# Performance work log

Measured on AMD Instinct MI355X. Metric: run time of the kernel, lower is better.

## Reference

```python
import jax, jax.numpy as jnp
import numpy as np

D_MODEL = 1024
N_HEAD = 16


def setup_inputs() -> dict:
    key = jax.random.key(0)
    ks = jax.random.split(key, 11)
    B, S, D = 2, 2048, D_MODEL
    scale = 1.0 / np.sqrt(D)
    inp = {
        "query_tensor": jax.random.normal(ks[0], (B, S, D), jnp.float32),
        "key_tensor": jax.random.normal(ks[1], (B, S, D), jnp.float32),
        "value_tensor": jax.random.normal(ks[2], (B, S, D), jnp.float32),
        "w_q": jax.random.normal(ks[3], (D, D), jnp.float32) * scale,
        "b_q": jnp.zeros((D,), jnp.float32),
        "w_k": jax.random.normal(ks[4], (D, D), jnp.float32) * scale,
        "b_k": jnp.zeros((D,), jnp.float32),
        "w_v": jax.random.normal(ks[5], (D, D), jnp.float32) * scale,
        "b_v": jnp.zeros((D,), jnp.float32),
        "w_out": jax.random.normal(ks[6], (D, D), jnp.float32) * scale,
        "b_out": jnp.zeros((D,), jnp.float32),
    }
    return inp


def _split_heads(x, n_head):
    b, s, d = x.shape
    return x.reshape(b, s, n_head, d // n_head).transpose(0, 2, 1, 3)  # [b,h,s,dk]


def reference(query_tensor, key_tensor, value_tensor, w_q, b_q, w_k, b_k, w_v, b_v, w_out, b_out):
    # torch Linear: y = x @ W.T + b
    q = query_tensor @ w_q.T + b_q
    k = key_tensor @ w_k.T + b_k
    v = value_tensor @ w_v.T + b_v
    q = _split_heads(q, N_HEAD)
    k = _split_heads(k, N_HEAD)
    v = _split_heads(v, N_HEAD)
    d_k = k.shape[-1]
    scores = jnp.einsum("bhqd,bhkd->bhqk", q, k) / jnp.sqrt(jnp.float32(d_k))
    attn = jax.nn.softmax(scores, axis=-1)
    ctx = jnp.einsum("bhqk,bhkd->bhqd", attn, v)
    b, h, s, dk = ctx.shape
    ctx = ctx.transpose(0, 2, 1, 3).reshape(b, s, h * dk)
    return ctx @ w_out.T + b_out
```

## Files before the change

### kernel.cpp

```cpp
#include <hip/hip_runtime.h>
#include <hip/hip_bf16.h>

using ushort = unsigned short;

typedef __attribute__((ext_vector_type(8))) short bf16x8;
typedef __attribute__((ext_vector_type(4))) float f32x4;
typedef __attribute__((ext_vector_type(16))) float f32x16;
typedef __attribute__((ext_vector_type(4))) unsigned short u16x4;

#define DEVINL __device__ __forceinline__


static constexpr size_t XQ_O = 0;
static constexpr size_t WQ_O = 12582912;
static constexpr size_t WO_O = 15728640;
static constexpr size_t QB_O = 16777216;
static constexpr size_t KB_O = 20971520;
static constexpr size_t VT_O = 25165824;
static constexpr size_t CTX_O = 0;

DEVINL ushort f2bf(float f) {
  unsigned u = __builtin_bit_cast(unsigned, f);
  u += 0x7fffu + ((u >> 16) & 1u);
  return (ushort)(u >> 16);
}

DEVINL void gld16(const ushort* g, ushort* lds) {
  __builtin_amdgcn_global_load_lds(
      (const __attribute__((address_space(1))) void*)g,
      (__attribute__((address_space(3))) void*)lds, 16, 0, 0);
}

__global__ __launch_bounds__(256) void cvt_all(
    const float* __restrict__ xq, const float* __restrict__ xk, const float* __restrict__ xv,
    const float* __restrict__ wq, const float* __restrict__ wk, const float* __restrict__ wv,
    const float* __restrict__ wo, ushort* __restrict__ ws)
{
  int e = (blockIdx.x * 256 + threadIdx.x) * 8;
  const float* s;
  if      (e < 4194304)  s = xq + e;
  else if (e < 8388608)  s = xk + (e - 4194304);
  else if (e < 12582912) s = xv + (e - 8388608);
  else if (e < 13631488) s = wq + (e - 12582912);
  else if (e < 14680064) s = wk + (e - 13631488);
  else if (e < 15728640) s = wv + (e - 14680064);
  else                   s = wo + (e - 15728640);
  float4 a = *(const float4*)s;
  float4 b = *(const float4*)(s + 4);
  union { u16x4 v; ushort u[4]; } r0, r1;
  r0.u[0] = f2bf(a.x); r0.u[1] = f2bf(a.y); r0.u[2] = f2bf(a.z); r0.u[3] = f2bf(a.w);
  r1.u[0] = f2bf(b.x); r1.u[1] = f2bf(b.y); r1.u[2] = f2bf(b.z); r1.u[3] = f2bf(b.w);
  *(u16x4*)(ws + e) = r0.v;
  *(u16x4*)(ws + e + 4) = r1.v;
}

template<int BN>
DEVINL void gemm_core(const ushort* __restrict__ A, const ushort* __restrict__ Bw,
                      const float* __restrict__ bias, void* __restrict__ Cout,
                      float scale, int omode, int row0, int col0)
{
  constexpr int K = 1024;
  constexpr int BI = BN / 32;
  constexpr int NJ = BN / 32;
  __shared__ ushort As[128 * 64];
  __shared__ ushort Bs[BN * 64];
  const int t = threadIdx.x;
  const int l = t & 63;
  const int w = t >> 6;
  const int wr = w >> 1, wc = w & 1;

  const int srow = t >> 3;
  const int scol8 = (t & 7) * 8;
  const int swz_half = ((((t & 7) * 16) ^ ((srow & 7) << 4)) >> 1);

  const ushort* Ap = A + (size_t)(row0 + srow) * K + scol8;
  const ushort* Bp = Bw + (size_t)(col0 + srow) * K + scol8;

  bf16x8 areg[4], breg[BI];
  auto loadstage = [&](int k0) {
#pragma unroll
    for (int i = 0; i < 4; ++i)
      areg[i] = *(const bf16x8*)(Ap + (size_t)(i * 32) * K + k0);
#pragma unroll
    for (int i = 0; i < BI; ++i)
      breg[i] = *(const bf16x8*)(Bp + (size_t)(i * 32) * K + k0);
  };

  f32x4 acc[4][NJ];
#pragma unroll
  for (int i = 0; i < 4; ++i)
#pragma unroll
    for (int j = 0; j < NJ; ++j) acc[i][j] = (f32x4){0.f, 0.f, 0.f, 0.f};

  loadstage(0);
#pragma unroll 1
  for (int kt = 0; kt < K / 64; ++kt) {
    __syncthreads();
#pragma unroll
    for (int i = 0; i < 4; ++i)
      *(bf16x8*)&As[(srow + i * 32) * 64 + swz_half] = areg[i];
#pragma unroll
    for (int i = 0; i < BI; ++i)
      *(bf16x8*)&Bs[(srow + i * 32) * 64 + swz_half] = breg[i];
    if (kt + 1 < K / 64) loadstage((kt + 1) * 64);
    __syncthreads();
#pragma unroll
    for (int ks = 0; ks < 2; ++ks) {
      bf16x8 af[4], bfr[NJ];
#pragma unroll
      for (int mi = 0; mi < 4; ++mi) {
        int r = wr * 64 + mi * 16 + (l & 15);
        int cb = ((ks << 6) | ((l >> 4) << 4)) ^ ((r & 7) << 4);
        af[mi] = *(const bf16x8*)&As[r * 64 + (cb >> 1)];
      }
#pragma unroll
      for (int nj = 0; nj < NJ; ++nj) {
        int r = wc * (BN / 2) + nj * 16 + (l & 15);
        int cb = ((ks << 6) | ((l >> 4) << 4)) ^ ((r & 7) << 4);
        bfr[nj] = *(const bf16x8*)&Bs[r * 64 + (cb >> 1)];
      }
#pragma unroll
      for (int mi = 0; mi < 4; ++mi)
#pragma unroll
        for (int nj = 0; nj < NJ; ++nj)
          acc[mi][nj] = __builtin_amdgcn_mfma_f32_16x16x32_bf16(af[mi], bfr[nj], acc[mi][nj], 0, 0, 0);
    }
  }

  const int cl = l & 15;
#pragma unroll
  for (int mi = 0; mi < 4; ++mi) {
#pragma unroll
    for (int nj = 0; nj < NJ; ++nj) {
      int n = col0 + wc * (BN / 2) + nj * 16 + cl;
      float bv = bias[n];
      int mbase = row0 + wr * 64 + mi * 16 + (l >> 4) * 4;
      if (omode == 1) {
        float* Of = (float*)Cout;
#pragma unroll
        for (int ri = 0; ri < 4; ++ri)
          Of[(size_t)(mbase + ri) * 1024 + n] = (acc[mi][nj][ri] + bv) * scale;
      } else if (omode == 0) {
        ushort* Ob = (ushort*)Cout;
        int h = n >> 6, d = n & 63;
#pragma unroll
        for (int ri = 0; ri < 4; ++ri) {
          int m = mbase + ri;
          int b = m >> 11, s = m & 2047;
          Ob[(size_t)((b * 16 + h) * 2048 + s) * 64 + d] = f2bf((acc[mi][nj][ri] + bv) * scale);
        }
      } else {
        ushort* Ob = (ushort*)Cout;
        int h = n >> 6, d = n & 63;
        int b = mbase >> 11, s = mbase & 2047;
        union { u16x4 v; ushort u[4]; } pk;
#pragma unroll
        for (int ri = 0; ri < 4; ++ri) pk.u[ri] = f2bf((acc[mi][nj][ri] + bv) * scale);
        *(u16x4*)&Ob[(size_t)((b * 16 + h) * 64 + d) * 2048 + s] = pk.v;
      }
    }
  }
}

__global__ __launch_bounds__(256, 2) void gemm_qkv(
    const ushort* __restrict__ ws_c, ushort* __restrict__ ws_m,
    const float* __restrict__ bq, const float* __restrict__ bk, const float* __restrict__ bv)
{
  const int z = blockIdx.z;
  const ushort* A = ws_c + XQ_O + (size_t)z * 4194304;
  const ushort* W = ws_c + WQ_O + (size_t)z * 1048576;
  const float* bias = (z == 0) ? bq : ((z == 1) ? bk : bv);
  ushort* dst = ws_m + QB_O + (size_t)z * 4194304;
  float scale = (z == 0) ? (0.125f * 1.4426950408889634f) : 1.0f;
  int omode = (z == 2) ? 2 : 0;
  gemm_core<128>(A, W, bias, dst, scale, omode, blockIdx.y * 128, blockIdx.x * 128);
}

__global__ __launch_bounds__(256, 2) void gemm_out(
    const ushort* __restrict__ ctx, const ushort* __restrict__ wo,
    const float* __restrict__ bo, float* __restrict__ out)
{
  gemm_core<64>(ctx, wo, bo, out, 1.0f, 1, blockIdx.y * 128, blockIdx.x * 64);
}

__global__ __launch_bounds__(512, 4) void attn8(
    const ushort* __restrict__ Qb, const ushort* __restrict__ Kb,
    const ushort* __restrict__ Vtb, ushort* __restrict__ Ctx)
{
  __shared__ ushort smem[32768];

  const int t = threadIdx.x, l = t & 63, w = t >> 6;
  const int wq4 = w & 3, half = w >> 2;
  const int hi2 = l >> 5, q = l & 31;

  const int hw = blockIdx.y * 16 + blockIdx.x;
  const int j = hw >> 3;
  const int bh = (hw & 7) + 8 * (j >> 4);
  const int qt = j & 15;

  const int kvb = half * 1024;
  const ushort* Qp = Qb + ((size_t)bh * 2048 + qt * 128 + wq4 * 32) * 64;
  const ushort* Kp = Kb + (size_t)bh * 2048 * 64;
  const ushort* Vp = Vtb + (size_t)bh * 64 * 2048;

  ushort* Ksh = smem + half * 8192;
  ushort* Vsh = smem + 16384 + half * 8192;

  bf16x8 qf[4];
#pragma unroll
  for (int ks = 0; ks < 4; ++ks)
    qf[ks] = *(const bf16x8*)(Qp + q * 64 + ks * 16 + hi2 * 8);

  auto stageKV = [&](int pp, int kv0) {
#pragma unroll
    for (int i = 0; i < 2; ++i) {
      int R = (i * 4 + wq4) * 8 + (l >> 3);
      int g = l & 7;
      int sR = (R & ~12) | ((R & 4) << 1) | ((R & 8) >> 1);
      gld16(Kp + (size_t)(kv0 + sR) * 64 + (g ^ (R & 7)) * 8,
            Ksh + pp * 4096 + (i * 4 + wq4) * 512);
      gld16(Vp + (size_t)R * 2048 + kv0 + (g ^ (R & 7)) * 8,
            Vsh + pp * 4096 + (i * 4 + wq4) * 512);
    }
  };

  f32x16 acc0, acc1;
#pragma unroll
  for (int i = 0; i < 16; ++i) { acc0[i] = 0.f; acc1[i] = 0.f; }
  f32x16 Zv;
#pragma unroll
  for (int i = 0; i < 16; ++i) Zv[i] = 0.f;
  float lrun = 0.f;

  const int rsw = (q & 7) << 4;

  stageKV(0, kvb);
  __syncthreads();

#pragma unroll 1
  for (int kt = 0; kt < 16; ++kt) {
    const int p = kt & 1;
    const ushort* Kl = Ksh + p * 4096;
    const ushort* Vl = Vsh + p * 4096;

    f32x16 scA, scB;
    __builtin_amdgcn_s_setprio(1);
    {
      bf16x8 kf = *(const bf16x8*)&Kl[q * 64 + (((hi2 * 16)) ^ rsw) / 2];
      scA = __builtin_amdgcn_mfma_f32_32x32x16_bf16(kf, qf[0], Zv, 0, 0, 0);
#pragma unroll
      for (int ks = 1; ks < 4; ++ks) {
        bf16x8 k2 = *(const bf16x8*)&Kl[q * 64 + (((ks * 32 + hi2 * 16) ^ rsw) >> 1)];
        scA = __builtin_amdgcn_mfma_f32_32x32x16_bf16(k2, qf[ks], scA, 0, 0, 0);
      }
      const int r1 = (32 + q) * 64;
      bf16x8 kg = *(const bf16x8*)&Kl[r1 + (((hi2 * 16)) ^ rsw) / 2];
      scB = __builtin_amdgcn_mfma_f32_32x32x16_bf16(kg, qf[0], Zv, 0, 0, 0);
#pragma unroll
      for (int ks = 1; ks < 4; ++ks) {
        bf16x8 k2 = *(const bf16x8*)&Kl[r1 + (((ks * 32 + hi2 * 16) ^ rsw) >> 1)];
        scB = __builtin_amdgcn_mfma_f32_32x32x16_bf16(k2, qf[ks], scB, 0, 0, 0);
      }
    }
    __builtin_amdgcn_s_setprio(0);

    if (kt + 1 < 16) stageKV(p ^ 1, kvb + (kt + 1) * 64);

#pragma unroll
    for (int c = 0; c < 2; ++c) {
      f32x16& sc = (c == 0) ? scA : scB;
      float s0 = 0.f, s1 = 0.f, s2 = 0.f, s3 = 0.f;
#pragma unroll
      for (int i = 0; i < 4; ++i) {
        float e0 = __builtin_amdgcn_exp2f(sc[i]);      sc[i] = e0;      s0 += e0;
        float e1 = __builtin_amdgcn_exp2f(sc[4 + i]);  sc[4 + i] = e1;  s1 += e1;
        float e2 = __builtin_amdgcn_exp2f(sc[8 + i]);  sc[8 + i] = e2;  s2 += e2;
        float e3 = __builtin_amdgcn_exp2f(sc[12 + i]); sc[12 + i] = e3; s3 += e3;
      }
      lrun += (s0 + s1) + (s2 + s3);

      union PU { bf16x8 v; unsigned u[4]; } pA, pB;
#pragma unroll
      for (int i = 0; i < 4; ++i) {
        asm("v_cvt_pk_bf16_f32 %0, %1, %2" : "=v"(pA.u[i]) : "v"(sc[2 * i]), "v"(sc[2 * i + 1]));
        asm("v_cvt_pk_bf16_f32 %0, %1, %2" : "=v"(pB.u[i]) : "v"(sc[8 + 2 * i]), "v"(sc[9 + 2 * i]));
      }

      __builtin_amdgcn_s_setprio(1);
#pragma unroll
      for (int db = 0; db < 2; ++db) {
        const int d = db * 32 + q;
        bf16x8 va = *(const bf16x8*)&Vl[d * 64 + (((c * 64 + hi2 * 16) ^ rsw) >> 1)];
        bf16x8 vb = *(const bf16x8*)&Vl[d * 64 + (((c * 64 + 32 + hi2 * 16) ^ rsw) >> 1)];
        if (db == 0) {
          acc0 = __builtin_amdgcn_mfma_f32_32x32x16_bf16(va, pA.v, acc0, 0, 0, 0);
          acc0 = __builtin_amdgcn_mfma_f32_32x32x16_bf16(vb, pB.v, acc0, 0, 0, 0);
        } else {
          acc1 = __builtin_amdgcn_mfma_f32_32x32x16_bf16(va, pA.v, acc1, 0, 0, 0);
          acc1 = __builtin_amdgcn_mfma_f32_32x32x16_bf16(vb, pB.v, acc1, 0, 0, 0);
        }
      }
      __builtin_amdgcn_s_setprio(0);
    }
    __syncthreads();
  }

  float lsum = lrun + __shfl_xor(lrun, 32);
  float* Lf = (float*)smem;

  if (l < 32) Lf[half * 128 + wq4 * 32 + q] = lsum;
  __syncthreads();
  const float inv = 1.0f / (Lf[wq4 * 32 + q] + Lf[128 + wq4 * 32 + q]);
  __syncthreads();

  auto mrg = [&](int row, int G) -> float* {
    return Lf + row * 64 + ((G ^ (row & 15)) << 2);
  };

  if (half == 1) {
    const int row = wq4 * 32 + q;
#pragma unroll
    for (int db = 0; db < 2; ++db)
#pragma unroll
      for (int g = 0; g < 4; ++g) {
        float4 v;
        if (db == 0) v = (float4){acc0[g * 4], acc0[g * 4 + 1], acc0[g * 4 + 2], acc0[g * 4 + 3]};
        else         v = (float4){acc1[g * 4], acc1[g * 4 + 1], acc1[g * 4 + 2], acc1[g * 4 + 3]};
        *(float4*)mrg(row, db * 8 + g * 2 + hi2) = v;
      }
  }
  __syncthreads();

  if (half == 0) {
    const int row = wq4 * 32 + q;
#pragma unroll
    for (int db = 0; db < 2; ++db)
#pragma unroll
      for (int g = 0; g < 4; ++g) {
        float* p = mrg(row, db * 8 + g * 2 + hi2);
        float4 pv = *(float4*)p;
        float4 o;
        if (db == 0) o = (float4){(acc0[g * 4] + pv.x) * inv, (acc0[g * 4 + 1] + pv.y) * inv,
                                  (acc0[g * 4 + 2] + pv.z) * inv, (acc0[g * 4 + 3] + pv.w) * inv};
        else         o = (float4){(acc1[g * 4] + pv.x) * inv, (acc1[g * 4 + 1] + pv.y) * inv,
                                  (acc1[g * 4 + 2] + pv.z) * inv, (acc1[g * 4 + 3] + pv.w) * inv};
        *(float4*)p = o;
      }
  }
  __syncthreads();

  {
    const int b = bh >> 4, h = bh & 15;
    const int d0 = (l & 7) * 8;
#pragma unroll
    for (int rr = 0; rr < 2; ++rr) {
      int row = w * 16 + rr * 8 + (l >> 3);
      float4 f0 = *(const float4*)mrg(row, (l & 7) * 2);
      float4 f1 = *(const float4*)mrg(row, (l & 7) * 2 + 1);
      union { u16x4 v; ushort u[4]; } o0, o1;
      o0.u[0] = f2bf(f0.x); o0.u[1] = f2bf(f0.y); o0.u[2] = f2bf(f0.z); o0.u[3] = f2bf(f0.w);
      o1.u[0] = f2bf(f1.x); o1.u[1] = f2bf(f1.y); o1.u[2] = f2bf(f1.z); o1.u[3] = f2bf(f1.w);
      ushort* dst = Ctx + ((size_t)b * 2048 + qt * 128 + row) * 1024 + h * 64 + d0;
      *(u16x4*)dst = o0.v;
      *(u16x4*)(dst + 4) = o1.v;
    }
  }
}

extern "C" void kernel_launch(void* const* d_in, const int* in_sizes, int n_in,
                              void* d_out, int out_size, void* d_ws, size_t ws_size,
                              hipStream_t stream) {
  const float* xq = (const float*)d_in[0];
  const float* xk = (const float*)d_in[1];
  const float* xv = (const float*)d_in[2];
  const float* wq = (const float*)d_in[3];
  const float* bq = (const float*)d_in[4];
  const float* wk = (const float*)d_in[5];
  const float* bk = (const float*)d_in[6];
  const float* wv = (const float*)d_in[7];
  const float* bv = (const float*)d_in[8];
  const float* wo = (const float*)d_in[9];
  const float* bo = (const float*)d_in[10];
  ushort* ws = (ushort*)d_ws;

  cvt_all<<<8192, 256, 0, stream>>>(xq, xk, xv, wq, wk, wv, wo, ws);
  gemm_qkv<<<dim3(8, 32, 3), 256, 0, stream>>>(ws, ws, bq, bk, bv);
  attn8<<<dim3(16, 32), 512, 0, stream>>>(ws + QB_O, ws + KB_O, ws + VT_O, ws + CTX_O);
  gemm_out<<<dim3(16, 32), 256, 0, stream>>>(ws + CTX_O, ws + WO_O, bo, (float*)d_out);
}
```

Measured before the change: 114.4 us.

## Restructure attention into 4-way KV split with 64 query rows per wave

The attention kernel now splits the KV sequence four ways across waves, and each wave handles 64 query rows (two 32-row MFMA tiles) instead of 32. Each K/V fragment read from LDS is therefore reused across two query tiles, which halves LDS reads per MFMA. K and V staging is divided between wave groups, with one loading K and the other loading V. This doubles LDS use to 128KB and the accumulator registers, so occupancy drops to 2 blocks per CU, and the final merge of four partial results takes more steps and barriers.

```diff
diff --git a/kernel.cpp b/kernel.cpp
--- a/kernel.cpp
+++ b/kernel.cpp
@@ -183,14 +183,14 @@
   gemm_core<64>(ctx, wo, bo, out, 1.0f, 1, blockIdx.y * 128, blockIdx.x * 64);
 }
 
-__global__ __launch_bounds__(512, 4) void attn8(
+__global__ __launch_bounds__(512, 2) void attn4k(
     const ushort* __restrict__ Qb, const ushort* __restrict__ Kb,
     const ushort* __restrict__ Vtb, ushort* __restrict__ Ctx)
 {
-  __shared__ ushort smem[32768];
+  __shared__ ushort smem[65536];
 
   const int t = threadIdx.x, l = t & 63, w = t >> 6;
-  const int wq4 = w & 3, half = w >> 2;
+  const int kq = w & 3, qw = w >> 2;
   const int hi2 = l >> 5, q = l & 31;
 
   const int hw = blockIdx.y * 16 + blockIdx.x;
@@ -198,92 +198,98 @@
   const int bh = (hw & 7) + 8 * (j >> 4);
   const int qt = j & 15;
 
-  const int kvb = half * 1024;
-  const ushort* Qp = Qb + ((size_t)bh * 2048 + qt * 128 + wq4 * 32) * 64;
+  const ushort* Qp = Qb + ((size_t)bh * 2048 + qt * 128 + qw * 64) * 64;
   const ushort* Kp = Kb + (size_t)bh * 2048 * 64;
   const ushort* Vp = Vtb + (size_t)bh * 64 * 2048;
 
-  ushort* Ksh = smem + half * 8192;
-  ushort* Vsh = smem + 16384 + half * 8192;
-
-  bf16x8 qf[4];
-#pragma unroll
-  for (int ks = 0; ks < 4; ++ks)
-    qf[ks] = *(const bf16x8*)(Qp + q * 64 + ks * 16 + hi2 * 8);
-
-  auto stageKV = [&](int pp, int kv0) {
-#pragma unroll
-    for (int i = 0; i < 2; ++i) {
-      int R = (i * 4 + wq4) * 8 + (l >> 3);
-      int g = l & 7;
-      int sR = (R & ~12) | ((R & 4) << 1) | ((R & 8) >> 1);
-      gld16(Kp + (size_t)(kv0 + sR) * 64 + (g ^ (R & 7)) * 8,
-            Ksh + pp * 4096 + (i * 4 + wq4) * 512);
-      gld16(Vp + (size_t)R * 2048 + kv0 + (g ^ (R & 7)) * 8,
-            Vsh + pp * 4096 + (i * 4 + wq4) * 512);
+  ushort* Ksh = smem + kq * 8192;
+  ushort* Vsh = smem + 32768 + kq * 8192;
+
+  bf16x8 qf[2][4];
+#pragma unroll
+  for (int qs = 0; qs < 2; ++qs)
+#pragma unroll
+    for (int ks = 0; ks < 4; ++ks)
+      qf[qs][ks] = *(const bf16x8*)(Qp + (qs * 32 + q) * 64 + ks * 16 + hi2 * 8);
+
+  auto stage = [&](int pp, int kv0) {
+    if (qw == 0) {
+#pragma unroll
+      for (int i = 0; i < 8; ++i) {
+        int R = i * 8 + (l >> 3);
+        int g = l & 7;
+        int sR = (R & ~12) | ((R & 4) << 1) | ((R & 8) >> 1);
+        gld16(Kp + (size_t)(kv0 + sR) * 64 + (g ^ (R & 7)) * 8,
+              Ksh + pp * 4096 + i * 512);
+      }
+    } else {
+#pragma unroll
+      for (int i = 0; i < 8; ++i) {
+        int R = i * 8 + (l >> 3);
+        int g = l & 7;
+        gld16(Vp + (size_t)R * 2048 + kv0 + (g ^ (R & 7)) * 8,
+              Vsh + pp * 4096 + i * 512);
+      }
     }
   };
 
-  f32x16 acc0, acc1;
-#pragma unroll
-  for (int i = 0; i < 16; ++i) { acc0[i] = 0.f; acc1[i] = 0.f; }
+  f32x16 acc[4];
   f32x16 Zv;
 #pragma unroll
   for (int i = 0; i < 16; ++i) Zv[i] = 0.f;
-  float lrun = 0.f;
+#pragma unroll
+  for (int a = 0; a < 4; ++a) acc[a] = Zv;
+  float lr0 = 0.f, lr1 = 0.f;
 
   const int rsw = (q & 7) << 4;
-
-  stageKV(0, kvb);
+  const int kvq = kq * 512;
+
+  stage(0, kvq);
   __syncthreads();
 
 #pragma unroll 1
-  for (int kt = 0; kt < 16; ++kt) {
+  for (int kt = 0; kt < 8; ++kt) {
     const int p = kt & 1;
     const ushort* Kl = Ksh + p * 4096;
     const ushort* Vl = Vsh + p * 4096;
 
-    f32x16 scA, scB;
-    __builtin_amdgcn_s_setprio(1);
-    {
-      bf16x8 kf = *(const bf16x8*)&Kl[q * 64 + (((hi2 * 16)) ^ rsw) / 2];
-      scA = __builtin_amdgcn_mfma_f32_32x32x16_bf16(kf, qf[0], Zv, 0, 0, 0);
+#pragma unroll
+    for (int c = 0; c < 2; ++c) {
+      bf16x8 kf[4];
+#pragma unroll
+      for (int ks = 0; ks < 4; ++ks)
+        kf[ks] = *(const bf16x8*)&Kl[(c * 32 + q) * 64 + (((ks * 32 + hi2 * 16) ^ rsw) >> 1)];
+      f32x16 s0, s1;
+      __builtin_amdgcn_s_setprio(1);
+      s0 = __builtin_amdgcn_mfma_f32_32x32x16_bf16(kf[0], qf[0][0], Zv, 0, 0, 0);
+      s1 = __builtin_amdgcn_mfma_f32_32x32x16_bf16(kf[0], qf[1][0], Zv, 0, 0, 0);
 #pragma unroll
       for (int ks = 1; ks < 4; ++ks) {
-        bf16x8 k2 = *(const bf16x8*)&Kl[q * 64 + (((ks * 32 + hi2 * 16) ^ rsw) >> 1)];
-        scA = __builtin_amdgcn_mfma_f32_32x32x16_bf16(k2, qf[ks], scA, 0, 0, 0);
-      }
-      const int r1 = (32 + q) * 64;
-      bf16x8 kg = *(const bf16x8*)&Kl[r1 + (((hi2 * 16)) ^ rsw) / 2];
-      scB = __builtin_amdgcn_mfma_f32_32x32x16_bf16(kg, qf[0], Zv, 0, 0, 0);
-#pragma unroll
-      for (int ks = 1; ks < 4; ++ks) {
-        bf16x8 k2 = *(const bf16x8*)&Kl[r1 + (((ks * 32 + hi2 * 16) ^ rsw) >> 1)];
-        scB = __builtin_amdgcn_mfma_f32_32x32x16_bf16(k2, qf[ks], scB, 0, 0, 0);
-      }
-    }
-    __builtin_amdgcn_s_setprio(0);
-
-    if (kt + 1 < 16) stageKV(p ^ 1, kvb + (kt + 1) * 64);
-
-#pragma unroll
-    for (int c = 0; c < 2; ++c) {
-      f32x16& sc = (c == 0) ? scA : scB;
-      float s0 = 0.f, s1 = 0.f, s2 = 0.f, s3 = 0.f;
+        s0 = __builtin_amdgcn_mfma_f32_32x32x16_bf16(kf[ks], qf[0][ks], s0, 0, 0, 0);
+        s1 = __builtin_amdgcn_mfma_f32_32x32x16_bf16(kf[ks], qf[1][ks], s1, 0, 0, 0);
+      }
+      __builtin_amdgcn_s_setprio(0);
+
+      if (c == 0 && kt < 7) stage(p ^ 1, kvq + (kt + 1) * 64);
+
+      float a0 = 0.f, a1 = 0.f, b0 = 0.f, b1 = 0.f;
+#pragma unroll
+      for (int i = 0; i < 8; ++i) {
+        float e0 = __builtin_amdgcn_exp2f(s0[i]);      s0[i] = e0;      a0 += e0;
+        float e1 = __builtin_amdgcn_exp2f(s0[8 + i]);  s0[8 + i] = e1;  a1 += e1;
+        float e2 = __builtin_amdgcn_exp2f(s1[i]);      s1[i] = e2;      b0 += e2;
+        float e3 = __builtin_amdgcn_exp2f(s1[8 + i]);  s1[8 + i] = e3;  b1 += e3;
+      }
+      lr0 += a0 + a1;
+      lr1 += b0 + b1;
+
+      union PU { bf16x8 v; unsigned u[4]; } pA0, pB0, pA1, pB1;
 #pragma unroll
       for (int i = 0; i < 4; ++i) {
-        float e0 = __builtin_amdgcn_exp2f(sc[i]);      sc[i] = e0;      s0 += e0;
-        float e1 = __builtin_amdgcn_exp2f(sc[4 + i]);  sc[4 + i] = e1;  s1 += e1;
-        float e2 = __builtin_amdgcn_exp2f(sc[8 + i]);  sc[8 + i] = e2;  s2 += e2;
-        float e3 = __builtin_amdgcn_exp2f(sc[12 + i]); sc[12 + i] = e3; s3 += e3;
-      }
-      lrun += (s0 + s1) + (s2 + s3);
-
-      union PU { bf16x8 v; unsigned u[4]; } pA, pB;
-#pragma unroll
-      for (int i = 0; i < 4; ++i) {
-        asm("v_cvt_pk_bf16_f32 %0, %1, %2" : "=v"(pA.u[i]) : "v"(sc[2 * i]), "v"(sc[2 * i + 1]));
-        asm("v_cvt_pk_bf16_f32 %0, %1, %2" : "=v"(pB.u[i]) : "v"(sc[8 + 2 * i]), "v"(sc[9 + 2 * i]));
+        asm("v_cvt_pk_bf16_f32 %0, %1, %2" : "=v"(pA0.u[i]) : "v"(s0[2 * i]), "v"(s0[2 * i + 1]));
+        asm("v_cvt_pk_bf16_f32 %0, %1, %2" : "=v"(pB0.u[i]) : "v"(s0[8 + 2 * i]), "v"(s0[9 + 2 * i]));
+        asm("v_cvt_pk_bf16_f32 %0, %1, %2" : "=v"(pA1.u[i]) : "v"(s1[2 * i]), "v"(s1[2 * i + 1]));
+        asm("v_cvt_pk_bf16_f32 %0, %1, %2" : "=v"(pB1.u[i]) : "v"(s1[8 + 2 * i]), "v"(s1[9 + 2 * i]));
       }
 
       __builtin_amdgcn_s_setprio(1);
@@ -292,75 +298,113 @@
         const int d = db * 32 + q;
         bf16x8 va = *(const bf16x8*)&Vl[d * 64 + (((c * 64 + hi2 * 16) ^ rsw) >> 1)];
         bf16x8 vb = *(const bf16x8*)&Vl[d * 64 + (((c * 64 + 32 + hi2 * 16) ^ rsw) >> 1)];
-        if (db == 0) {
-          acc0 = __builtin_amdgcn_mfma_f32_32x32x16_bf16(va, pA.v, acc0, 0, 0, 0);
-          acc0 = __builtin_amdgcn_mfma_f32_32x32x16_bf16(vb, pB.v, acc0, 0, 0, 0);
-        } else {
-          acc1 = __builtin_amdgcn_mfma_f32_32x32x16_bf16(va, pA.v, acc1, 0, 0, 0);
-          acc1 = __builtin_amdgcn_mfma_f32_32x32x16_bf16(vb, pB.v, acc1, 0, 0, 0);
+        acc[db]     = __builtin_amdgcn_mfma_f32_32x32x16_bf16(va, pA0.v, acc[db], 0, 0, 0);
+        acc[db]     = __builtin_amdgcn_mfma_f32_32x32x16_bf16(vb, pB0.v, acc[db], 0, 0, 0);
+        acc[2 + db] = __builtin_amdgcn_mfma_f32_32x32x16_bf16(va, pA1.v, acc[2 + db], 0, 0, 0);
+        acc[2 + db] = __builtin_amdgcn_mfma_f32_32x32x16_bf16(vb, pB1.v, acc[2 + db], 0, 0, 0);
+      }
+      __builtin_amdgcn_s_setprio(0);
+    }
+    __syncthreads();
+  }
+
+  float ls0 = lr0 + __shfl_xor(lr0, 32);
+  float ls1 = lr1 + __shfl_xor(lr1, 32);
+  float* Lf = (float*)smem;
+  if (l < 32) {
+    Lf[16384 + kq * 128 + qw * 64 + q] = ls0;
+    Lf[16384 + kq * 128 + qw * 64 + 32 + q] = ls1;
+  }
+  __syncthreads();
+  const float inv0 = 1.0f / (Lf[16384 + qw * 64 + q] + Lf[16384 + 128 + qw * 64 + q] +
+                             Lf[16384 + 256 + qw * 64 + q] + Lf[16384 + 384 + qw * 64 + q]);
+  const float inv1 = 1.0f / (Lf[16384 + qw * 64 + 32 + q] + Lf[16384 + 128 + qw * 64 + 32 + q] +
+                             Lf[16384 + 256 + qw * 64 + 32 + q] + Lf[16384 + 384 + qw * 64 + 32 + q]);
+  __syncthreads();
+
+  auto mrg = [&](float* base, int row, int slot) -> float* {
+    return base + row * 64 + ((slot ^ (row & 15)) << 2);
+  };
+
+  if (kq == 1 || kq == 3) {
+    float* Rg = Lf + ((kq == 1) ? 0 : 8192) + qw * 4096;
+#pragma unroll
+    for (int qs = 0; qs < 2; ++qs)
+#pragma unroll
+      for (int db = 0; db < 2; ++db)
+#pragma unroll
+        for (int g = 0; g < 4; ++g) {
+          float4 v = (float4){acc[qs * 2 + db][g * 4], acc[qs * 2 + db][g * 4 + 1],
+                              acc[qs * 2 + db][g * 4 + 2], acc[qs * 2 + db][g * 4 + 3]};
+          *(float4*)mrg(Rg, qs * 32 + q, db * 8 + g * 2 + hi2) = v;
         }
-      }
-      __builtin_amdgcn_s_setprio(0);
-    }
-    __syncthreads();
-  }
-
-  float lsum = lrun + __shfl_xor(lrun, 32);
-  float* Lf = (float*)smem;
-
-  if (l < 32) Lf[half * 128 + wq4 * 32 + q] = lsum;
-  __syncthreads();
-  const float inv = 1.0f / (Lf[wq4 * 32 + q] + Lf[128 + wq4 * 32 + q]);
-  __syncthreads();
-
-  auto mrg = [&](int row, int G) -> float* {
-    return Lf + row * 64 + ((G ^ (row & 15)) << 2);
-  };
-
-  if (half == 1) {
-    const int row = wq4 * 32 + q;
-#pragma unroll
-    for (int db = 0; db < 2; ++db)
-#pragma unroll
-      for (int g = 0; g < 4; ++g) {
-        float4 v;
-        if (db == 0) v = (float4){acc0[g * 4], acc0[g * 4 + 1], acc0[g * 4 + 2], acc0[g * 4 + 3]};
-        else         v = (float4){acc1[g * 4], acc1[g * 4 + 1], acc1[g * 4 + 2], acc1[g * 4 + 3]};
-        *(float4*)mrg(row, db * 8 + g * 2 + hi2) = v;
-      }
-  }
-  __syncthreads();
-
-  if (half == 0) {
-    const int row = wq4 * 32 + q;
-#pragma unroll
-    for (int db = 0; db < 2; ++db)
-#pragma unroll
-      for (int g = 0; g < 4; ++g) {
-        float* p = mrg(row, db * 8 + g * 2 + hi2);
-        float4 pv = *(float4*)p;
-        float4 o;
-        if (db == 0) o = (float4){(acc0[g * 4] + pv.x) * inv, (acc0[g * 4 + 1] + pv.y) * inv,
-                                  (acc0[g * 4 + 2] + pv.z) * inv, (acc0[g * 4 + 3] + pv.w) * inv};
-        else         o = (float4){(acc1[g * 4] + pv.x) * inv, (acc1[g * 4 + 1] + pv.y) * inv,
-                                  (acc1[g * 4 + 2] + pv.z) * inv, (acc1[g * 4 + 3] + pv.w) * inv};
-        *(float4*)p = o;
-      }
+  }
+  __syncthreads();
+
+  if (kq == 0) {
+    float* Rg = Lf + qw * 4096;
+#pragma unroll
+    for (int qs = 0; qs < 2; ++qs)
+#pragma unroll
+      for (int db = 0; db < 2; ++db)
+#pragma unroll
+        for (int g = 0; g < 4; ++g) {
+          float4 v = *(float4*)mrg(Rg, qs * 32 + q, db * 8 + g * 2 + hi2);
+          acc[qs * 2 + db][g * 4] += v.x;     acc[qs * 2 + db][g * 4 + 1] += v.y;
+          acc[qs * 2 + db][g * 4 + 2] += v.z; acc[qs * 2 + db][g * 4 + 3] += v.w;
+        }
+  } else if (kq == 2) {
+    float* Rg = Lf + 8192 + qw * 4096;
+#pragma unroll
+    for (int qs = 0; qs < 2; ++qs)
+#pragma unroll
+      for (int db = 0; db < 2; ++db)
+#pragma unroll
+        for (int g = 0; g < 4; ++g) {
+          float* p = mrg(Rg, qs * 32 + q, db * 8 + g * 2 + hi2);
+          float4 v = *(float4*)p;
+          v.x += acc[qs * 2 + db][g * 4];     v.y += acc[qs * 2 + db][g * 4 + 1];
+          v.z += acc[qs * 2 + db][g * 4 + 2]; v.w += acc[qs * 2 + db][g * 4 + 3];
+          *(float4*)p = v;
+        }
+  }
+  __syncthreads();
+
+  if (kq == 0) {
+    float* R2g = Lf + 8192 + qw * 4096;
+    float* R1g = Lf + qw * 4096;
+#pragma unroll
+    for (int qs = 0; qs < 2; ++qs) {
+      const float inv = (qs == 0) ? inv0 : inv1;
+#pragma unroll
+      for (int db = 0; db < 2; ++db)
+#pragma unroll
+        for (int g = 0; g < 4; ++g) {
+          float4 v = *(float4*)mrg(R2g, qs * 32 + q, db * 8 + g * 2 + hi2);
+          float4 o = (float4){(acc[qs * 2 + db][g * 4] + v.x) * inv,
+                              (acc[qs * 2 + db][g * 4 + 1] + v.y) * inv,
+                              (acc[qs * 2 + db][g * 4 + 2] + v.z) * inv,
+                              (acc[qs * 2 + db][g * 4 + 3] + v.w) * inv};
+          *(float4*)mrg(R1g, qs * 32 + q, db * 8 + g * 2 + hi2) = o;
+        }
+    }
   }
   __syncthreads();
 
   {
     const int b = bh >> 4, h = bh & 15;
-    const int d0 = (l & 7) * 8;
 #pragma unroll
     for (int rr = 0; rr < 2; ++rr) {
-      int row = w * 16 + rr * 8 + (l >> 3);
-      float4 f0 = *(const float4*)mrg(row, (l & 7) * 2);
-      float4 f1 = *(const float4*)mrg(row, (l & 7) * 2 + 1);
+      int row128 = w * 16 + rr * 8 + (l >> 3);
+      float* base = Lf + (row128 >> 6) * 4096;
+      int row64 = row128 & 63;
+      int G = (l & 7) * 2;
+      float4 f0 = *(float4*)mrg(base, row64, G);
+      float4 f1 = *(float4*)mrg(base, row64, G + 1);
       union { u16x4 v; ushort u[4]; } o0, o1;
       o0.u[0] = f2bf(f0.x); o0.u[1] = f2bf(f0.y); o0.u[2] = f2bf(f0.z); o0.u[3] = f2bf(f0.w);
       o1.u[0] = f2bf(f1.x); o1.u[1] = f2bf(f1.y); o1.u[2] = f2bf(f1.z); o1.u[3] = f2bf(f1.w);
-      ushort* dst = Ctx + ((size_t)b * 2048 + qt * 128 + row) * 1024 + h * 64 + d0;
+      ushort* dst = Ctx + ((size_t)b * 2048 + qt * 128 + row128) * 1024 + h * 64 + (l & 7) * 8;
       *(u16x4*)dst = o0.v;
       *(u16x4*)(dst + 4) = o1.v;
     }
@@ -385,6 +429,6 @@
 
   cvt_all<<<8192, 256, 0, stream>>>(xq, xk, xv, wq, wk, wv, wo, ws);
   gemm_qkv<<<dim3(8, 32, 3), 256, 0, stream>>>(ws, ws, bq, bk, bv);
-  attn8<<<dim3(16, 32), 512, 0, stream>>>(ws + QB_O, ws + KB_O, ws + VT_O, ws + CTX_O);
+  attn4k<<<dim3(16, 32), 512, 0, stream>>>(ws + QB_O, ws + KB_O, ws + VT_O, ws + CTX_O);
   gemm_out<<<dim3(16, 32), 256, 0, stream>>>(ws + CTX_O, ws + WO_O, bo, (float*)d_out);
 }
```

Result: slower. 119.3 us (+4.3%).
